# Kernel tuning notes

Hardware: AMD Instinct MI355X
Metric: run time of the kernel (lower is better)

Reference implementation:

```python
import jax, jax.numpy as jnp
import numpy as np

N_NODES = 50000
N_EDGES = 800000
D_IN = 96
D_OUT = 96
K_ORDER = 3


def setup_inputs() -> dict:
    key = jax.random.key(0)
    k1, k2, k3, k4, k5 = jax.random.split(key, 5)
    rows = jax.random.randint(k1, (N_EDGES,), 0, N_NODES, dtype=jnp.int64 if jax.config.jax_enable_x64 else jnp.int32)
    cols = jax.random.randint(k2, (N_EDGES,), 0, N_NODES, dtype=jnp.int64 if jax.config.jax_enable_x64 else jnp.int32)
    vals = jax.random.uniform(k3, (N_EDGES,), dtype=jnp.float32) * (1.0 / 16.0)  # ~sym-normalized weights
    H = jax.random.normal(k4, (N_NODES, D_IN), dtype=jnp.float32)
    W = jax.random.normal(k5, (D_IN, D_OUT), dtype=jnp.float32) * (1.0 / np.sqrt(D_IN))
    bias = jnp.zeros((D_OUT,), dtype=jnp.float32)
    return {"rows": rows, "cols": cols, "vals": vals, "H": H, "W": W, "bias": bias}


def reference(rows, cols, vals, H, W, bias):
    n = H.shape[0]

    def spmm(X):  # L @ X via gather-multiply-scatter over COO edges
        return jax.ops.segment_sum(vals[:, None] * X[cols], rows, num_segments=n)

    def ln_mm(X):  # (2L - I) @ X
        return 2.0 * spmm(X) - X

    # k = 0 term: T_0 = H
    H_out = H @ W
    # k = 1 term: T_1 = (2L - I) H  (differentiable, as in torch code)
    T_prev = H
    T_curr = ln_mm(H)
    H_out = H_out + T_curr @ W
    # k >= 2: recurrence computed under no_grad in the original -> stop_gradient
    for _ in range(2, K_ORDER + 1):
        T_next = jax.lax.stop_gradient(2.0 * ln_mm(T_curr) - T_prev)
        H_out = H_out + T_next @ W
        T_prev, T_curr = T_curr, T_next
    return H_out + bias
```

## Files before the change

### kernel.cpp

```cpp
#include <hip/hip_runtime.h>
#include <hip/hip_fp16.h>

#define NN 50000
#define NE 800000
#define D  96
#define NB_SCAN 196
#define N4 (NN * D / 4)
#define CB4 ((N4 + 255) / 256)
#define WFRAG_BLKS 5

typedef unsigned int   uint32;
typedef unsigned short uint16;
typedef short v8s __attribute__((ext_vector_type(8)));
typedef float v4f __attribute__((ext_vector_type(4)));

__device__ inline uint16 f32_to_bf16(float f) {
    uint32 u = __float_as_uint(f);
    u += 0x7FFF + ((u >> 16) & 1);
    return (uint16)(u >> 16);
}
__device__ inline float bf16_to_f32(uint16 h) {
    return __uint_as_float(((uint32)h) << 16);
}

__global__ void prep(const float4* __restrict__ H, ushort4* __restrict__ Hb,
                     const float* __restrict__ W, uint16* __restrict__ Wfrag,
                     int* __restrict__ counts) {
    int b = blockIdx.x;
    int t = threadIdx.x;
    if (b < CB4) {
        int i = b * 256 + t;
        if (i < N4) {
            float4 v = H[i];
            ushort4 o;
            o.x = f32_to_bf16(v.x); o.y = f32_to_bf16(v.y);
            o.z = f32_to_bf16(v.z); o.w = f32_to_bf16(v.w);
            Hb[i] = o;
        }
    } else if (b < CB4 + NB_SCAN) {
        int i = (b - CB4) * 256 + t;
        if (i < NN) counts[i] = 0;
    } else {
        int idx = (b - CB4 - NB_SCAN) * 256 + t;
        if (idx < 18 * 64) {
            int bt = idx >> 6, lane = idx & 63;
            int nt = bt / 3, kc = bt % 3;
            int col = nt * 16 + (lane & 15);
            int kbase = kc * 32 + (lane >> 4) * 8;
            uint16 tmp[8];
            #pragma unroll
            for (int j = 0; j < 8; ++j) tmp[j] = f32_to_bf16(W[(kbase + j) * D + col]);
            uint32* dst = (uint32*)(Wfrag + ((size_t)bt * 64 + lane) * 8);
            const uint32* src = (const uint32*)tmp;
            #pragma unroll
            for (int j = 0; j < 4; ++j) dst[j] = src[j];
        }
    }
}

__global__ void hist_slots(const int* __restrict__ rows, int* __restrict__ counts,
                           int* __restrict__ slot) {
    int e = blockIdx.x * blockDim.x + threadIdx.x;
    if (e < NE) slot[e] = atomicAdd(&counts[rows[e]], 1);
}

__global__ void scan_p1(const int* __restrict__ counts, int* __restrict__ partials) {
    __shared__ int red[256];
    int t = threadIdx.x;
    int i = blockIdx.x * 256 + t;
    red[t] = (i < NN) ? counts[i] : 0;
    __syncthreads();
    for (int off = 128; off > 0; off >>= 1) {
        if (t < off) red[t] += red[t + off];
        __syncthreads();
    }
    if (t == 0) partials[blockIdx.x] = red[0];
}

__global__ void scan_p23(const int* __restrict__ counts, const int* __restrict__ partials,
                         int* __restrict__ row_ptr) {
    __shared__ int pp[256];
    __shared__ int sh[256];
    int t = threadIdx.x;
    pp[t] = (t < NB_SCAN) ? partials[t] : 0;
    __syncthreads();
    for (int off = 1; off < 256; off <<= 1) {
        int u = (t >= off) ? pp[t - off] : 0;
        __syncthreads();
        pp[t] += u;
        __syncthreads();
    }
    int blk_off = (blockIdx.x == 0) ? 0 : pp[blockIdx.x - 1];
    int i = blockIdx.x * 256 + t;
    int v = (i < NN) ? counts[i] : 0;
    sh[t] = v;
    __syncthreads();
    for (int off = 1; off < 256; off <<= 1) {
        int u = (t >= off) ? sh[t - off] : 0;
        __syncthreads();
        sh[t] += u;
        __syncthreads();
    }
    int excl = sh[t] - v + blk_off;
    if (i < NN) row_ptr[i] = excl;
    if (i == NN - 1) row_ptr[NN] = excl + v;
}

__global__ void fill_edges(const int* __restrict__ rows, const int* __restrict__ cols,
                           const float* __restrict__ vals, const int* __restrict__ row_ptr,
                           const int* __restrict__ slot, uint32* __restrict__ edges) {
    int e = blockIdx.x * blockDim.x + threadIdx.x;
    if (e < NE) {
        int p = row_ptr[rows[e]] + slot[e];
        __half_raw hr = __half_raw(__float2half(vals[e]));
        edges[p] = (uint32)(cols[e] & 0xFFFF) | ((uint32)hr.x << 16);
    }
}

__global__ void spmm(const int* __restrict__ row_ptr, const uint32* __restrict__ edges,
                     const uint16* __restrict__ Xb, const uint16* __restrict__ A,
                     const uint16* __restrict__ B, uint16* __restrict__ Yb,
                     float scale, float ca, float cb, int n_nodes) {
    int tid  = threadIdx.x;
    int lane = tid & 31;
    int g    = tid >> 5;
    int r = blockIdx.x * 8 + g;
    if (r >= n_nodes) return;
    bool act = lane < 24;

    float4 acc = make_float4(0.f, 0.f, 0.f, 0.f);
    if (act) {
        ushort4 av = ((const ushort4*)(A + (size_t)r * D))[lane];
        ushort4 bv = ((const ushort4*)(B + (size_t)r * D))[lane];
        acc.x = ca * bf16_to_f32(av.x) + cb * bf16_to_f32(bv.x);
        acc.y = ca * bf16_to_f32(av.y) + cb * bf16_to_f32(bv.y);
        acc.z = ca * bf16_to_f32(av.z) + cb * bf16_to_f32(bv.z);
        acc.w = ca * bf16_to_f32(av.w) + cb * bf16_to_f32(bv.w);
    }

    int s = row_ptr[r];
    int e = row_ptr[r + 1];
    int i = s;
    for (; i + 3 < e; i += 4) {
        uint32 e0 = edges[i], e1 = edges[i+1], e2 = edges[i+2], e3 = edges[i+3];
        ushort4 x0, x1, x2, x3;
        x0.x=x0.y=x0.z=x0.w=0; x1=x0; x2=x0; x3=x0;
        if (act) {
            x0 = ((const ushort4*)(Xb + (size_t)(e0 & 0xFFFF) * D))[lane];
            x1 = ((const ushort4*)(Xb + (size_t)(e1 & 0xFFFF) * D))[lane];
            x2 = ((const ushort4*)(Xb + (size_t)(e2 & 0xFFFF) * D))[lane];
            x3 = ((const ushort4*)(Xb + (size_t)(e3 & 0xFFFF) * D))[lane];
        }
        __half_raw h0, h1, h2, h3;
        h0.x = (uint16)(e0 >> 16); h1.x = (uint16)(e1 >> 16);
        h2.x = (uint16)(e2 >> 16); h3.x = (uint16)(e3 >> 16);
        float v0 = scale * __half2float(__half(h0));
        float v1 = scale * __half2float(__half(h1));
        float v2 = scale * __half2float(__half(h2));
        float v3 = scale * __half2float(__half(h3));
        acc.x += v0*bf16_to_f32(x0.x) + v1*bf16_to_f32(x1.x) + v2*bf16_to_f32(x2.x) + v3*bf16_to_f32(x3.x);
        acc.y += v0*bf16_to_f32(x0.y) + v1*bf16_to_f32(x1.y) + v2*bf16_to_f32(x2.y) + v3*bf16_to_f32(x3.y);
        acc.z += v0*bf16_to_f32(x0.z) + v1*bf16_to_f32(x1.z) + v2*bf16_to_f32(x2.z) + v3*bf16_to_f32(x3.z);
        acc.w += v0*bf16_to_f32(x0.w) + v1*bf16_to_f32(x1.w) + v2*bf16_to_f32(x2.w) + v3*bf16_to_f32(x3.w);
    }
    for (; i < e; ++i) {
        uint32 e0 = edges[i];
        __half_raw h0; h0.x = (uint16)(e0 >> 16);
        float v0 = scale * __half2float(__half(h0));
        if (act) {
            ushort4 x0 = ((const ushort4*)(Xb + (size_t)(e0 & 0xFFFF) * D))[lane];
            acc.x += v0 * bf16_to_f32(x0.x);
            acc.y += v0 * bf16_to_f32(x0.y);
            acc.z += v0 * bf16_to_f32(x0.z);
            acc.w += v0 * bf16_to_f32(x0.w);
        }
    }
    if (act) {
        ushort4 ob;
        ob.x = f32_to_bf16(acc.x); ob.y = f32_to_bf16(acc.y);
        ob.z = f32_to_bf16(acc.z); ob.w = f32_to_bf16(acc.w);
        ((ushort4*)(Yb + (size_t)r * D))[lane] = ob;
    }
}

__global__ void mfma_gemm(const uint16* __restrict__ Sb, const uint16* __restrict__ Wfrag,
                          const float* __restrict__ bias, float* __restrict__ out) {
    int tid   = threadIdx.x;
    int lane  = tid & 63;
    int wv    = blockIdx.x * (blockDim.x >> 6) + (tid >> 6);
    int nwv   = gridDim.x * (blockDim.x >> 6);
    int col   = lane & 15;
    int quad  = lane >> 4;

    v8s wf[6][3];
    #pragma unroll
    for (int nt = 0; nt < 6; ++nt)
        #pragma unroll
        for (int kc = 0; kc < 3; ++kc)
            wf[nt][kc] = ((const v8s*)Wfrag)[(nt * 3 + kc) * 64 + lane];

    float bi[6];
    #pragma unroll
    for (int nt = 0; nt < 6; ++nt) bi[nt] = bias[nt * 16 + col];

    for (int s = wv; s < NN / 16; s += nwv) {
        int r0 = s * 16;
        const uint16* arow = Sb + (size_t)(r0 + col) * D + quad * 8;
        v8s a0 = *((const v8s*)(arow));
        v8s a1 = *((const v8s*)(arow + 32));
        v8s a2 = *((const v8s*)(arow + 64));
        v4f acc[6];
        #pragma unroll
        for (int nt = 0; nt < 6; ++nt) {
            v4f c = {0.f, 0.f, 0.f, 0.f};
            c = __builtin_amdgcn_mfma_f32_16x16x32_bf16(a0, wf[nt][0], c, 0, 0, 0);
            c = __builtin_amdgcn_mfma_f32_16x16x32_bf16(a1, wf[nt][1], c, 0, 0, 0);
            c = __builtin_amdgcn_mfma_f32_16x16x32_bf16(a2, wf[nt][2], c, 0, 0, 0);
            acc[nt] = c;
        }
        #pragma unroll
        for (int nt = 0; nt < 6; ++nt) {
            float* o = out + (size_t)(r0 + quad * 4) * D + nt * 16 + col;
            o[0 * D] = acc[nt][0] + bi[nt];
            o[1 * D] = acc[nt][1] + bi[nt];
            o[2 * D] = acc[nt][2] + bi[nt];
            o[3 * D] = acc[nt][3] + bi[nt];
        }
    }
}

extern "C" void kernel_launch(void* const* d_in, const int* in_sizes, int n_in,
                              void* d_out, int out_size, void* d_ws, size_t ws_size,
                              hipStream_t stream) {
    const int*   rows = (const int*)d_in[0];
    const int*   cols = (const int*)d_in[1];
    const float* vals = (const float*)d_in[2];
    const float* H    = (const float*)d_in[3];
    const float* W    = (const float*)d_in[4];
    const float* bias = (const float*)d_in[5];
    float* out = (float*)d_out;

    char* ws = (char*)d_ws;
    uint16* Hb       = (uint16*)ws;  ws += (size_t)NN * D * 2;
    uint16* T1b      = (uint16*)ws;  ws += (size_t)NN * D * 2;
    uint16* T2b      = (uint16*)ws;  ws += (size_t)NN * D * 2;
    uint32* edges    = (uint32*)ws;  ws += (size_t)NE * 4;
    uint16* Wfrag    = (uint16*)ws;  ws += (size_t)18 * 64 * 8 * 2;
    int*    counts   = (int*)ws;     ws += (size_t)NN * 4;
    int*    row_ptr  = (int*)ws;     ws += (size_t)(NN + 1) * 4;
    int*    partials = (int*)ws;     ws += 256 * 4;
    int*    slot     = (int*)T2b;
    uint16* Sb       = T1b;

    const int eb = (NE + 255) / 256;

    prep<<<CB4 + NB_SCAN + WFRAG_BLKS, 256, 0, stream>>>(
        (const float4*)H, (ushort4*)Hb, W, Wfrag, counts);
    hist_slots<<<eb, 256, 0, stream>>>(rows, counts, slot);
    scan_p1<<<NB_SCAN, 256, 0, stream>>>(counts, partials);
    scan_p23<<<NB_SCAN, 256, 0, stream>>>(counts, partials, row_ptr);
    fill_edges<<<eb, 256, 0, stream>>>(rows, cols, vals, row_ptr, slot, edges);

    const int sb = (NN + 7) / 8;

    spmm<<<sb, 256, 0, stream>>>(row_ptr, edges, Hb, Hb, Hb, T1b, 2.0f, -1.0f, 0.0f, NN);
    spmm<<<sb, 256, 0, stream>>>(row_ptr, edges, T1b, T1b, Hb, T2b, 4.0f, -2.0f, -1.0f, NN);
    spmm<<<sb, 256, 0, stream>>>(row_ptr, edges, T2b, Hb, T2b, Sb, 4.0f, 1.0f, -1.0f, NN);
    mfma_gemm<<<391, 256, 0, stream>>>(Sb, Wfrag, bias, out);
}
```

Measured before the change: 240.7 us.

## Drop slot array via cursor atomics; unroll SpMM gather by eight with nontemporal I/O

```diff
diff --git a/kernel.cpp b/kernel.cpp
--- a/kernel.cpp
+++ b/kernel.cpp
@@ -11,16 +11,26 @@
 
 typedef unsigned int   uint32;
 typedef unsigned short uint16;
-typedef short v8s __attribute__((ext_vector_type(8)));
-typedef float v4f __attribute__((ext_vector_type(4)));
+typedef short  v8s __attribute__((ext_vector_type(8)));
+typedef float  v4f __attribute__((ext_vector_type(4)));
+typedef unsigned int v2u __attribute__((ext_vector_type(2)));
 
 __device__ inline uint16 f32_to_bf16(float f) {
     uint32 u = __float_as_uint(f);
     u += 0x7FFF + ((u >> 16) & 1);
     return (uint16)(u >> 16);
 }
-__device__ inline float bf16_to_f32(uint16 h) {
-    return __uint_as_float(((uint32)h) << 16);
+
+__device__ inline void u2f(v2u u, float& a, float& b, float& c, float& d) {
+    a = __uint_as_float(u.x << 16);
+    b = __uint_as_float(u.x & 0xFFFF0000u);
+    c = __uint_as_float(u.y << 16);
+    d = __uint_as_float(u.y & 0xFFFF0000u);
+}
+
+__device__ inline float f16_val(uint32 e) {
+    __half_raw h; h.x = (uint16)(e >> 16);
+    return __half2float(__half(h));
 }
 
 __global__ void prep(const float4* __restrict__ H, ushort4* __restrict__ Hb,
@@ -58,10 +68,9 @@
     }
 }
 
-__global__ void hist_slots(const int* __restrict__ rows, int* __restrict__ counts,
-                           int* __restrict__ slot) {
+__global__ void hist(const int* __restrict__ rows, int* __restrict__ counts) {
     int e = blockIdx.x * blockDim.x + threadIdx.x;
-    if (e < NE) slot[e] = atomicAdd(&counts[rows[e]], 1);
+    if (e < NE) atomicAdd(&counts[rows[e]], 1);
 }
 
 __global__ void scan_p1(const int* __restrict__ counts, int* __restrict__ partials) {
@@ -77,7 +86,7 @@
     if (t == 0) partials[blockIdx.x] = red[0];
 }
 
-__global__ void scan_p23(const int* __restrict__ counts, const int* __restrict__ partials,
+__global__ void scan_p23(int* __restrict__ counts, const int* __restrict__ partials,
                          int* __restrict__ row_ptr) {
     __shared__ int pp[256];
     __shared__ int sh[256];
@@ -102,16 +111,16 @@
         __syncthreads();
     }
     int excl = sh[t] - v + blk_off;
-    if (i < NN) row_ptr[i] = excl;
+    if (i < NN) { row_ptr[i] = excl; counts[i] = excl; }
     if (i == NN - 1) row_ptr[NN] = excl + v;
 }
 
 __global__ void fill_edges(const int* __restrict__ rows, const int* __restrict__ cols,
-                           const float* __restrict__ vals, const int* __restrict__ row_ptr,
-                           const int* __restrict__ slot, uint32* __restrict__ edges) {
+                           const float* __restrict__ vals, int* __restrict__ cursor,
+                           uint32* __restrict__ edges) {
     int e = blockIdx.x * blockDim.x + threadIdx.x;
     if (e < NE) {
-        int p = row_ptr[rows[e]] + slot[e];
+        int p = atomicAdd(&cursor[rows[e]], 1);
         __half_raw hr = __half_raw(__float2half(vals[e]));
         edges[p] = (uint32)(cols[e] & 0xFFFF) | ((uint32)hr.x << 16);
     }
@@ -120,67 +129,74 @@
 __global__ void spmm(const int* __restrict__ row_ptr, const uint32* __restrict__ edges,
                      const uint16* __restrict__ Xb, const uint16* __restrict__ A,
                      const uint16* __restrict__ B, uint16* __restrict__ Yb,
-                     float scale, float ca, float cb, int n_nodes) {
+                     float scale, float ca, float cb) {
     int tid  = threadIdx.x;
     int lane = tid & 31;
     int g    = tid >> 5;
     int r = blockIdx.x * 8 + g;
-    if (r >= n_nodes) return;
-    bool act = lane < 24;
-
-    float4 acc = make_float4(0.f, 0.f, 0.f, 0.f);
-    if (act) {
-        ushort4 av = ((const ushort4*)(A + (size_t)r * D))[lane];
-        ushort4 bv = ((const ushort4*)(B + (size_t)r * D))[lane];
-        acc.x = ca * bf16_to_f32(av.x) + cb * bf16_to_f32(bv.x);
-        acc.y = ca * bf16_to_f32(av.y) + cb * bf16_to_f32(bv.y);
-        acc.z = ca * bf16_to_f32(av.z) + cb * bf16_to_f32(bv.z);
-        acc.w = ca * bf16_to_f32(av.w) + cb * bf16_to_f32(bv.w);
-    }
+    if (r >= NN) return;
+    if (lane >= 24) return;
+
+    const v2u* xbase = (const v2u*)Xb;
+
+    v2u av = __builtin_nontemporal_load((const v2u*)(A + (size_t)r * D) + lane);
+    v2u bv = __builtin_nontemporal_load((const v2u*)(B + (size_t)r * D) + lane);
+    float a0,a1,a2,a3,b0,b1,b2,b3;
+    u2f(av, a0,a1,a2,a3);
+    u2f(bv, b0,b1,b2,b3);
+    float ax = ca*a0 + cb*b0;
+    float ay = ca*a1 + cb*b1;
+    float az = ca*a2 + cb*b2;
+    float aw = ca*a3 + cb*b3;
 
     int s = row_ptr[r];
     int e = row_ptr[r + 1];
     int i = s;
+    for (; i + 7 < e; i += 8) {
+        uint32 ee[8];
+        #pragma unroll
+        for (int j = 0; j < 8; ++j) ee[j] = edges[i + j];
+        v2u xx[8];
+        #pragma unroll
+        for (int j = 0; j < 8; ++j)
+            xx[j] = xbase[(size_t)(ee[j] & 0xFFFF) * 24 + lane];
+        #pragma unroll
+        for (int j = 0; j < 8; ++j) {
+            float v = scale * f16_val(ee[j]);
+            float x0,x1,x2,x3;
+            u2f(xx[j], x0,x1,x2,x3);
+            ax += v*x0; ay += v*x1; az += v*x2; aw += v*x3;
+        }
+    }
     for (; i + 3 < e; i += 4) {
-        uint32 e0 = edges[i], e1 = edges[i+1], e2 = edges[i+2], e3 = edges[i+3];
-        ushort4 x0, x1, x2, x3;
-        x0.x=x0.y=x0.z=x0.w=0; x1=x0; x2=x0; x3=x0;
-        if (act) {
-            x0 = ((const ushort4*)(Xb + (size_t)(e0 & 0xFFFF) * D))[lane];
-            x1 = ((const ushort4*)(Xb + (size_t)(e1 & 0xFFFF) * D))[lane];
-            x2 = ((const ushort4*)(Xb + (size_t)(e2 & 0xFFFF) * D))[lane];
-            x3 = ((const ushort4*)(Xb + (size_t)(e3 & 0xFFFF) * D))[lane];
-        }
-        __half_raw h0, h1, h2, h3;
-        h0.x = (uint16)(e0 >> 16); h1.x = (uint16)(e1 >> 16);
-        h2.x = (uint16)(e2 >> 16); h3.x = (uint16)(e3 >> 16);
-        float v0 = scale * __half2float(__half(h0));
-        float v1 = scale * __half2float(__half(h1));
-        float v2 = scale * __half2float(__half(h2));
-        float v3 = scale * __half2float(__half(h3));
-        acc.x += v0*bf16_to_f32(x0.x) + v1*bf16_to_f32(x1.x) + v2*bf16_to_f32(x2.x) + v3*bf16_to_f32(x3.x);
-        acc.y += v0*bf16_to_f32(x0.y) + v1*bf16_to_f32(x1.y) + v2*bf16_to_f32(x2.y) + v3*bf16_to_f32(x3.y);
-        acc.z += v0*bf16_to_f32(x0.z) + v1*bf16_to_f32(x1.z) + v2*bf16_to_f32(x2.z) + v3*bf16_to_f32(x3.z);
-        acc.w += v0*bf16_to_f32(x0.w) + v1*bf16_to_f32(x1.w) + v2*bf16_to_f32(x2.w) + v3*bf16_to_f32(x3.w);
+        uint32 ee[4];
+        #pragma unroll
+        for (int j = 0; j < 4; ++j) ee[j] = edges[i + j];
+        v2u xx[4];
+        #pragma unroll
+        for (int j = 0; j < 4; ++j)
+            xx[j] = xbase[(size_t)(ee[j] & 0xFFFF) * 24 + lane];
+        #pragma unroll
+        for (int j = 0; j < 4; ++j) {
+            float v = scale * f16_val(ee[j]);
+            float x0,x1,x2,x3;
+            u2f(xx[j], x0,x1,x2,x3);
+            ax += v*x0; ay += v*x1; az += v*x2; aw += v*x3;
+        }
     }
     for (; i < e; ++i) {
         uint32 e0 = edges[i];
-        __half_raw h0; h0.x = (uint16)(e0 >> 16);
-        float v0 = scale * __half2float(__half(h0));
-        if (act) {
-            ushort4 x0 = ((const ushort4*)(Xb + (size_t)(e0 & 0xFFFF) * D))[lane];
-            acc.x += v0 * bf16_to_f32(x0.x);
-            acc.y += v0 * bf16_to_f32(x0.y);
-            acc.z += v0 * bf16_to_f32(x0.z);
-            acc.w += v0 * bf16_to_f32(x0.w);
-        }
-    }
-    if (act) {
-        ushort4 ob;
-        ob.x = f32_to_bf16(acc.x); ob.y = f32_to_bf16(acc.y);
-        ob.z = f32_to_bf16(acc.z); ob.w = f32_to_bf16(acc.w);
-        ((ushort4*)(Yb + (size_t)r * D))[lane] = ob;
-    }
+        float v = scale * f16_val(e0);
+        v2u x = xbase[(size_t)(e0 & 0xFFFF) * 24 + lane];
+        float x0,x1,x2,x3;
+        u2f(x, x0,x1,x2,x3);
+        ax += v*x0; ay += v*x1; az += v*x2; aw += v*x3;
+    }
+
+    v2u o;
+    o.x = (uint32)f32_to_bf16(ax) | ((uint32)f32_to_bf16(ay) << 16);
+    o.y = (uint32)f32_to_bf16(az) | ((uint32)f32_to_bf16(aw) << 16);
+    __builtin_nontemporal_store(o, (v2u*)(Yb + (size_t)r * D) + lane);
 }
 
 __global__ void mfma_gemm(const uint16* __restrict__ Sb, const uint16* __restrict__ Wfrag,
@@ -249,22 +265,21 @@
     int*    counts   = (int*)ws;     ws += (size_t)NN * 4;
     int*    row_ptr  = (int*)ws;     ws += (size_t)(NN + 1) * 4;
     int*    partials = (int*)ws;     ws += 256 * 4;
-    int*    slot     = (int*)T2b;
     uint16* Sb       = T1b;
 
     const int eb = (NE + 255) / 256;
 
     prep<<<CB4 + NB_SCAN + WFRAG_BLKS, 256, 0, stream>>>(
         (const float4*)H, (ushort4*)Hb, W, Wfrag, counts);
-    hist_slots<<<eb, 256, 0, stream>>>(rows, counts, slot);
+    hist<<<eb, 256, 0, stream>>>(rows, counts);
     scan_p1<<<NB_SCAN, 256, 0, stream>>>(counts, partials);
     scan_p23<<<NB_SCAN, 256, 0, stream>>>(counts, partials, row_ptr);
-    fill_edges<<<eb, 256, 0, stream>>>(rows, cols, vals, row_ptr, slot, edges);
+    fill_edges<<<eb, 256, 0, stream>>>(rows, cols, vals, counts, edges);
 
     const int sb = (NN + 7) / 8;
 
-    spmm<<<sb, 256, 0, stream>>>(row_ptr, edges, Hb, Hb, Hb, T1b, 2.0f, -1.0f, 0.0f, NN);
-    spmm<<<sb, 256, 0, stream>>>(row_ptr, edges, T1b, T1b, Hb, T2b, 4.0f, -2.0f, -1.0f, NN);
-    spmm<<<sb, 256, 0, stream>>>(row_ptr, edges, T2b, Hb, T2b, Sb, 4.0f, 1.0f, -1.0f, NN);
+    spmm<<<sb, 256, 0, stream>>>(row_ptr, edges, Hb, Hb, Hb, T1b, 2.0f, -1.0f, 0.0f);
+    spmm<<<sb, 256, 0, stream>>>(row_ptr, edges, T1b, T1b, Hb, T2b, 4.0f, -2.0f, -1.0f);
+    spmm<<<sb, 256, 0, stream>>>(row_ptr, edges, T2b, Hb, T2b, Sb, 4.0f, 1.0f, -1.0f);
     mfma_gemm<<<391, 256, 0, stream>>>(Sb, Wfrag, bias, out);
 }
```

New measurement: 278.0 us. 15.5% more time.
